# Performance work log

Measured on AMD Instinct MI355X. Metric: run time of the kernel, lower is better.

Reference implementation:

```python
import jax, jax.numpy as jnp
import numpy as np

L_RTN = 3  # complex taps produced by the RTN head (w_rtn3 out dim = 2*L_RTN)
EPS = 1e-12


def _to_complex(x):
    # (B, 2n) real interleaved [re0, im0, re1, im1, ...] -> (B, n) complex
    return x[:, 0::2] + 1j * x[:, 1::2]


def _to_real(xc):
    # (B, n) complex -> (B, 2n) real interleaved
    b, n = xc.shape
    return jnp.stack([xc.real, xc.imag], axis=-1).reshape(b, 2 * n)


def _complex_conv_taps(h_c, x_c):
    # per-sample causal complex FIR: out[t] = sum_l h[l] * x[t-l]
    # h_c: (B, L) complex, x_c: (B, n) complex
    n = x_c.shape[1]
    out = jnp.zeros_like(x_c)
    for l in range(h_c.shape[1]):  # L is tiny and static
        shifted = jnp.pad(x_c, ((0, 0), (l, 0)))[:, :n]
        out = out + h_c[:, l:l + 1] * shifted
    return out


def setup_inputs() -> dict:
    key = jax.random.key(0)
    ks = jax.random.split(key, 16)
    B, D_IN, H1, CH, H_RTN, H2, D_OUT = 8192, 512, 4096, 256, 1024, 4096, 512
    s = 0.02  # weight init scale
    x = jax.random.normal(ks[0], (B, D_IN), jnp.float32)
    w1 = s * jax.random.normal(ks[1], (H1, D_IN), jnp.float32)
    b1 = jnp.zeros((H1,), jnp.float32)
    w2 = s * jax.random.normal(ks[2], (CH, H1), jnp.float32)
    b2 = jnp.zeros((CH,), jnp.float32)
    w_rtn1 = s * jax.random.normal(ks[3], (H_RTN, CH), jnp.float32)
    b_rtn1 = jnp.zeros((H_RTN,), jnp.float32)
    w_rtn2 = s * jax.random.normal(ks[4], (H_RTN, H_RTN), jnp.float32)
    b_rtn2 = jnp.zeros((H_RTN,), jnp.float32)
    w_rtn3 = s * jax.random.normal(ks[5], (2 * L_RTN, H_RTN), jnp.float32)
    # bias so that RTN starts near identity tap [1, 0, 0, ...]
    b_rtn3 = jnp.zeros((2 * L_RTN,), jnp.float32).at[0].set(1.0)
    w3 = s * jax.random.normal(ks[6], (H2, CH), jnp.float32)
    b3 = jnp.zeros((H2,), jnp.float32)
    w4 = s * jax.random.normal(ks[7], (D_OUT, H2), jnp.float32)
    b4 = jnp.zeros((D_OUT,), jnp.float32)
    h = jax.random.normal(ks[8], (2,), jnp.float32)
    h = h / jnp.linalg.norm(h)  # unit-power single-tap fading channel
    noise = 0.1 * jax.random.normal(ks[9], (B, CH), jnp.float32)
    return {"x": x, "w1": w1, "b1": b1, "w2": w2, "b2": b2,
            "w_rtn1": w_rtn1, "b_rtn1": b_rtn1, "w_rtn2": w_rtn2,
            "b_rtn2": b_rtn2, "w_rtn3": w_rtn3, "b_rtn3": b_rtn3,
            "w3": w3, "b3": b3, "w4": w4, "b4": b4, "h": h, "noise": noise}


def reference(x, w1, b1, w2, b2, w_rtn1, b_rtn1, w_rtn2, b_rtn2,
              w_rtn3, b_rtn3, w3, b3, w4, b4, h, noise):
    # encoder (linear1 -> relu -> linear2)
    a = jax.nn.relu(x @ w1.T + b1)
    s = a @ w2.T + b2                      # (B, 2n) channel signal
    # power normalization: sqrt(2n) * sqrt(0.5) * s / ||s||
    scale = jnp.sqrt(s.shape[1] * 0.5)
    s = scale * s / jnp.linalg.norm(s, axis=1, keepdims=True)
    tx_c = _to_complex(s)                  # (B, n) transmitted symbols
    # single-tap complex channel
    h_c = h[0] + 1j * h[1]
    y = _to_real(h_c * tx_c) + noise       # add per-sample AWGN
    y_c = _to_complex(y)
    # LS channel estimate (1 tap): h_est = <y, x> / <x, x>
    num = jnp.sum(y_c * jnp.conj(tx_c), axis=1, keepdims=True)
    den = jnp.sum(jnp.abs(tx_c) ** 2, axis=1, keepdims=True)
    h_est = num / den                      # (B, 1)
    # zero-forcing signal estimate
    x_eq = y_c * jnp.conj(h_est) / (jnp.abs(h_est) ** 2 + EPS)
    xr = _to_real(x_eq)                    # (B, 2n)
    # RTN: predict inverse taps and apply per-sample complex conv
    g = jnp.tanh(xr @ w_rtn1.T + b_rtn1)
    g = jnp.tanh(g @ w_rtn2.T + b_rtn2)
    h_inv = g @ w_rtn3.T + b_rtn3          # (B, 2*L_RTN)
    h_inv_c = h_inv[:, 0::2] + 1j * h_inv[:, 1::2]
    xr = _to_real(_complex_conv_taps(h_inv_c, _to_complex(xr)))
    # decoder (linear3 -> relu -> linear4)
    out = jax.nn.relu(xr @ w3.T + b3)
    return out @ w4.T + b4
```

## Files before the change

### kernel.cpp

```cpp
#include <hip/hip_runtime.h>
#include <hip/hip_bf16.h>
#include <math.h>

using bf16 = __hip_bfloat16;
typedef __attribute__((ext_vector_type(8))) short short8;
typedef __attribute__((ext_vector_type(4))) float float4v;

template <typename T> __device__ inline T cvt_out(float v);
template <> __device__ inline float cvt_out<float>(float v) { return v; }
template <> __device__ inline bf16 cvt_out<bf16>(float v) { return __float2bfloat16(v); }

__device__ inline void gload_lds16(const bf16* g, bf16* l) {
    __builtin_amdgcn_global_load_lds(
        (const __attribute__((address_space(1))) void*)g,
        (__attribute__((address_space(3))) void*)l, 16, 0, 0);
}

struct CvtPack {
    const float* src[7];
    bf16* dst[7];
    int end[7];
};

__global__ __launch_bounds__(256) void cvt_all(CvtPack p) {
    int e = (blockIdx.x * 256 + threadIdx.x) * 4;
    int start = 0;
#pragma unroll
    for (int s = 0; s < 7; ++s) {
        if (e < p.end[s]) {
            int off = e - start;
            float4 v = *(const float4*)(p.src[s] + off);
            bf16* d = p.dst[s] + off;
            d[0] = __float2bfloat16(v.x);
            d[1] = __float2bfloat16(v.y);
            d[2] = __float2bfloat16(v.z);
            d[3] = __float2bfloat16(v.w);
            return;
        }
        start = p.end[s];
    }
}

__device__ inline float4 load4f(const float* p) { return *(const float4*)p; }
__device__ inline float4 load4f(const bf16* p) {
    ushort4 u = *(const ushort4*)p;
    float4 r;
    r.x = __uint_as_float((unsigned)u.x << 16);
    r.y = __uint_as_float((unsigned)u.y << 16);
    r.z = __uint_as_float((unsigned)u.z << 16);
    r.w = __uint_as_float((unsigned)u.w << 16);
    return r;
}
__device__ inline void store4(float* p, float4 v) { *(float4*)p = v; }
__device__ inline void store4(bf16* p, float4 v) {
    p[0] = __float2bfloat16(v.x); p[1] = __float2bfloat16(v.y);
    p[2] = __float2bfloat16(v.z); p[3] = __float2bfloat16(v.w);
}

template <int NK, int ACT, typename InT, typename OutT>
__global__ __launch_bounds__(256) void reduceK(const InT* __restrict__ p,
                                               const float* __restrict__ bias,
                                               OutT* __restrict__ out,
                                               size_t mn, int nmask, int total4) {
    int i = blockIdx.x * 256 + threadIdx.x;
    if (i < total4) {
        int idx = i * 4;
        float4 r = *(const float4*)(bias + (idx & nmask));
#pragma unroll
        for (int k = 0; k < NK; ++k) {
            float4 a = load4f(p + k * mn + idx);
            r.x += a.x; r.y += a.y; r.z += a.z; r.w += a.w;
        }
        if (ACT == 1) {
            r.x = fmaxf(r.x, 0.f); r.y = fmaxf(r.y, 0.f);
            r.z = fmaxf(r.z, 0.f); r.w = fmaxf(r.w, 0.f);
        } else if (ACT == 2) {
            r.x = tanhf(r.x); r.y = tanhf(r.y);
            r.z = tanhf(r.z); r.w = tanhf(r.w);
        }
        store4(out + idx, r);
    }
}

template <int ACT, typename OutT, int WMT, int WNT, int BKT, bool PARTIAL>
__global__ __launch_bounds__(256) void gemm_bt(const bf16* __restrict__ A,
                                               const bf16* __restrict__ W,
                                               const float* __restrict__ bias,
                                               OutT* __restrict__ C,
                                               int M, int N, int K,
                                               int nbn, int kcount) {
    constexpr int TBM = 32 * WMT;
    constexpr int TBN = 32 * WNT;
    constexpr int CPR = BKT / 8;
    constexpr int CA = TBM * CPR;
    constexpr int CB = TBN * CPR;

    __shared__ bf16 As[TBM * BKT];
    __shared__ bf16 Bs[TBN * BKT];

    const int bi = blockIdx.x;
    const int xcd = bi & 7, t = bi >> 3;
    const int bn = t % nbn;
    const int bm = xcd + 8 * (t / nbn);
    const int kbeg = PARTIAL ? blockIdx.y * kcount : 0;
    OutT* Cp = PARTIAL ? C + (size_t)blockIdx.y * M * N : C;

    const int tid = threadIdx.x;
    const int wave = tid >> 6, lane = tid & 63;
    const int wm = (wave >> 1) * (16 * WMT), wn = (wave & 1) * (16 * WNT);
    const int quad = lane >> 4, lrow = lane & 15;

    float4v acc[WMT][WNT] = {};
    const size_t arow = (size_t)(bm * TBM) * K;
    const size_t brow = (size_t)(bn * TBN) * K;

    for (int k0 = kbeg; k0 < kbeg + kcount; k0 += BKT) {
        __syncthreads();
#pragma unroll
        for (int tt = 0; tt < CA / 256; ++tt) {
            int base = tt * 256 + wave * 64;
            int c = base + lane;
            int row = c / CPR, col = (c % CPR) * 8;
            gload_lds16(A + arow + (size_t)row * K + k0 + col, As + base * 8);
        }
#pragma unroll
        for (int tt = 0; tt < CB / 256; ++tt) {
            int base = tt * 256 + wave * 64;
            int c = base + lane;
            int row = c / CPR, col = (c % CPR) * 8;
            gload_lds16(W + brow + (size_t)row * K + k0 + col, Bs + base * 8);
        }
        __syncthreads();
#pragma unroll
        for (int kk = 0; kk < BKT; kk += 32) {
            short8 af[WMT], bfr[WNT];
#pragma unroll
            for (int i = 0; i < WMT; ++i)
                af[i] = *(const short8*)(As + (wm + i * 16 + lrow) * BKT + kk + quad * 8);
#pragma unroll
            for (int j = 0; j < WNT; ++j)
                bfr[j] = *(const short8*)(Bs + (wn + j * 16 + lrow) * BKT + kk + quad * 8);
#pragma unroll
            for (int i = 0; i < WMT; ++i)
#pragma unroll
                for (int j = 0; j < WNT; ++j)
                    acc[i][j] = __builtin_amdgcn_mfma_f32_16x16x32_bf16(af[i], bfr[j], acc[i][j], 0, 0, 0);
        }
    }

#pragma unroll
    for (int i = 0; i < WMT; ++i) {
        int m0 = bm * TBM + wm + i * 16 + quad * 4;
#pragma unroll
        for (int j = 0; j < WNT; ++j) {
            int n = bn * TBN + wn + j * 16 + lrow;
            if constexpr (PARTIAL) {
#pragma unroll
                for (int r = 0; r < 4; ++r)
                    Cp[(size_t)(m0 + r) * N + n] = cvt_out<OutT>(acc[i][j][r]);
            } else {
                float bv = bias[n];
#pragma unroll
                for (int r = 0; r < 4; ++r) {
                    float v = acc[i][j][r] + bv;
                    if (ACT == 1) v = fmaxf(v, 0.f);
                    else if (ACT == 2) v = tanhf(v);
                    Cp[(size_t)(m0 + r) * N + n] = cvt_out<OutT>(v);
                }
            }
        }
    }
}

template <int ACT, typename OutT>
__global__ __launch_bounds__(512, 4) void gemm_bt_wide(const bf16* __restrict__ A,
                                                       const bf16* __restrict__ W,
                                                       const float* __restrict__ bias,
                                                       OutT* __restrict__ C,
                                                       int M, int N, int K,
                                                       int nbn) {
    constexpr int TBM = 256, TBN = 128, BKT = 64;
    constexpr int CPR = BKT / 8;
    constexpr int CA = TBM * CPR;
    constexpr int CB = TBN * CPR;

    __shared__ bf16 As[TBM * BKT];
    __shared__ bf16 Bs[TBN * BKT];

    const int bi = blockIdx.x;
    const int xcd = bi & 7, t = bi >> 3;
    const int bn = t % nbn;
    const int bm = xcd + 8 * (t / nbn);

    const int tid = threadIdx.x;
    const int wave = tid >> 6, lane = tid & 63;
    const int wm = (wave >> 1) * 64, wn = (wave & 1) * 64;
    const int quad = lane >> 4, lrow = lane & 15;

    float4v acc[4][4] = {};
    const size_t arow = (size_t)(bm * TBM) * K;
    const size_t brow = (size_t)(bn * TBN) * K;

    for (int k0 = 0; k0 < K; k0 += BKT) {
        __syncthreads();
#pragma unroll
        for (int tt = 0; tt < CA / 512; ++tt) {
            int base = tt * 512 + wave * 64;
            int c = base + lane;
            int row = c / CPR, col = (c % CPR) * 8;
            gload_lds16(A + arow + (size_t)row * K + k0 + col, As + base * 8);
        }
#pragma unroll
        for (int tt = 0; tt < CB / 512; ++tt) {
            int base = tt * 512 + wave * 64;
            int c = base + lane;
            int row = c / CPR, col = (c % CPR) * 8;
            gload_lds16(W + brow + (size_t)row * K + k0 + col, Bs + base * 8);
        }
        __syncthreads();
#pragma unroll
        for (int kk = 0; kk < BKT; kk += 32) {
            short8 af[4], bfr[4];
#pragma unroll
            for (int i = 0; i < 4; ++i)
                af[i] = *(const short8*)(As + (wm + i * 16 + lrow) * BKT + kk + quad * 8);
#pragma unroll
            for (int j = 0; j < 4; ++j)
                bfr[j] = *(const short8*)(Bs + (wn + j * 16 + lrow) * BKT + kk + quad * 8);
#pragma unroll
            for (int i = 0; i < 4; ++i)
#pragma unroll
                for (int j = 0; j < 4; ++j)
                    acc[i][j] = __builtin_amdgcn_mfma_f32_16x16x32_bf16(af[i], bfr[j], acc[i][j], 0, 0, 0);
        }
    }

#pragma unroll
    for (int i = 0; i < 4; ++i) {
        int m0 = bm * TBM + wm + i * 16 + quad * 4;
#pragma unroll
        for (int j = 0; j < 4; ++j) {
            int n = bn * TBN + wn + j * 16 + lrow;
            float bv = bias[n];
#pragma unroll
            for (int r = 0; r < 4; ++r) {
                float v = acc[i][j][r] + bv;
                if (ACT == 1) v = fmaxf(v, 0.f);
                else if (ACT == 2) v = tanhf(v);
                C[(size_t)(m0 + r) * N + n] = cvt_out<OutT>(v);
            }
        }
    }
}

__global__ __launch_bounds__(64) void channel_kernel(const float* __restrict__ s,
                                                     const float* __restrict__ h,
                                                     const float* __restrict__ noise,
                                                     float* __restrict__ xr_f,
                                                     bf16* __restrict__ xr_b) {
    const int b = blockIdx.x, lane = threadIdx.x;
    const float* srow = s + (size_t)b * 256;

    float ss = 0.f;
#pragma unroll
    for (int t = 0; t < 4; ++t) {
        float v = srow[lane + 64 * t];
        ss += v * v;
    }
#pragma unroll
    for (int off = 32; off; off >>= 1) ss += __shfl_xor(ss, off);
    const float inv = sqrtf(128.0f) / sqrtf(ss);

    const float hre = h[0], him = h[1];

    float yre[2], yim[2];
    float nre = 0.f, nim = 0.f, den = 0.f;
#pragma unroll
    for (int t = 0; t < 2; ++t) {
        int c = lane + 64 * t;
        float tr = srow[2 * c] * inv, ti = srow[2 * c + 1] * inv;
        float yr = hre * tr - him * ti + noise[(size_t)b * 256 + 2 * c];
        float yi = hre * ti + him * tr + noise[(size_t)b * 256 + 2 * c + 1];
        yre[t] = yr; yim[t] = yi;
        nre += yr * tr + yi * ti;
        nim += yi * tr - yr * ti;
        den += tr * tr + ti * ti;
    }
#pragma unroll
    for (int off = 32; off; off >>= 1) {
        nre += __shfl_xor(nre, off);
        nim += __shfl_xor(nim, off);
        den += __shfl_xor(den, off);
    }
    const float her = nre / den, hei = nim / den;
    const float d2 = her * her + hei * hei + 1e-12f;

#pragma unroll
    for (int t = 0; t < 2; ++t) {
        int c = lane + 64 * t;
        float xre = (yre[t] * her + yim[t] * hei) / d2;
        float xim = (yim[t] * her - yre[t] * hei) / d2;
        xr_f[(size_t)b * 256 + 2 * c] = xre;
        xr_f[(size_t)b * 256 + 2 * c + 1] = xim;
        xr_b[(size_t)b * 256 + 2 * c] = __float2bfloat16(xre);
        xr_b[(size_t)b * 256 + 2 * c + 1] = __float2bfloat16(xim);
    }
}

__global__ __launch_bounds__(64) void rtn_taps_conv(const bf16* __restrict__ g2,
                                                    const float* __restrict__ wr3,
                                                    const float* __restrict__ br3,
                                                    const float* __restrict__ xr_f,
                                                    bf16* __restrict__ xr2) {
    const int b = blockIdx.x, lane = threadIdx.x;
    const bf16* grow = g2 + (size_t)b * 1024;

    float acc[6] = {0.f, 0.f, 0.f, 0.f, 0.f, 0.f};
#pragma unroll
    for (int t = 0; t < 16; ++t) {
        int k = lane + 64 * t;
        float gv = __bfloat162float(grow[k]);
#pragma unroll
        for (int j = 0; j < 6; ++j) acc[j] += gv * wr3[j * 1024 + k];
    }
#pragma unroll
    for (int j = 0; j < 6; ++j)
#pragma unroll
        for (int off = 32; off; off >>= 1) acc[j] += __shfl_xor(acc[j], off);

    float tre[3], tim[3];
#pragma unroll
    for (int l = 0; l < 3; ++l) {
        tre[l] = acc[2 * l] + br3[2 * l];
        tim[l] = acc[2 * l + 1] + br3[2 * l + 1];
    }

    const float* xrow = xr_f + (size_t)b * 256;
#pragma unroll
    for (int t = 0; t < 2; ++t) {
        int c = lane + 64 * t;
        float ore = 0.f, oim = 0.f;
#pragma unroll
        for (int l = 0; l < 3; ++l) {
            int cc = c - l;
            if (cc >= 0) {
                float xre = xrow[2 * cc], xim = xrow[2 * cc + 1];
                ore += tre[l] * xre - tim[l] * xim;
                oim += tre[l] * xim + tim[l] * xre;
            }
        }
        xr2[(size_t)b * 256 + 2 * c] = __float2bfloat16(ore);
        xr2[(size_t)b * 256 + 2 * c + 1] = __float2bfloat16(oim);
    }
}

extern "C" void kernel_launch(void* const* d_in, const int* in_sizes, int n_in,
                              void* d_out, int out_size, void* d_ws, size_t ws_size,
                              hipStream_t stream) {
    constexpr int B = 8192, D_IN = 512, H1 = 4096, CH = 256, HR = 1024, H2 = 4096, DOUT = 512;

    const float* x   = (const float*)d_in[0];
    const float* w1  = (const float*)d_in[1];
    const float* b1  = (const float*)d_in[2];
    const float* w2  = (const float*)d_in[3];
    const float* b2  = (const float*)d_in[4];
    const float* wr1 = (const float*)d_in[5];
    const float* br1 = (const float*)d_in[6];
    const float* wr2 = (const float*)d_in[7];
    const float* br2 = (const float*)d_in[8];
    const float* wr3 = (const float*)d_in[9];
    const float* br3 = (const float*)d_in[10];
    const float* w3  = (const float*)d_in[11];
    const float* b3  = (const float*)d_in[12];
    const float* w4  = (const float*)d_in[13];
    const float* b4  = (const float*)d_in[14];
    const float* h   = (const float*)d_in[15];
    const float* noise = (const float*)d_in[16];

    char* ws = (char*)d_ws;
    bf16*  a    = (bf16*)(ws + 0);
    float* sF   = (float*)(ws + 0);
    bf16*  g1   = (bf16*)(ws + 0);
    bf16*  g2   = (bf16*)(ws + 16777216);
    bf16*  tbuf = (bf16*)(ws + 0);
    bf16*  w1B  = (bf16*)(ws + 67108864);
    bf16*  w2B  = (bf16*)(ws + 71303168);
    bf16*  wr1B = (bf16*)(ws + 73400320);
    bf16*  wr2B = (bf16*)(ws + 73924608);
    bf16*  w3B  = (bf16*)(ws + 76021760);
    bf16*  w4B  = (bf16*)(ws + 78118912);
    bf16*  xB   = (bf16*)(ws + 82313216);
    bf16*  g2P  = (bf16*)(ws + 82313216);
    float* xrF  = (float*)(ws + 99090432);
    bf16*  xrB  = (bf16*)(ws + 107479040);
    bf16*  xr2  = (bf16*)(ws + 111673344);
    bf16*  g6P  = (bf16*)(ws + 82313216);

    dim3 blk(256);

    CvtPack p;
    const float* srcs[7] = {x, w1, w2, wr1, wr2, w3, w4};
    bf16* dsts[7] = {xB, w1B, w2B, wr1B, wr2B, w3B, w4B};
    int ns[7] = {B * D_IN, H1 * D_IN, CH * H1, HR * CH, HR * HR, H2 * CH, DOUT * H2};
    int cum = 0;
    for (int i = 0; i < 7; ++i) { p.src[i] = srcs[i]; p.dst[i] = dsts[i]; cum += ns[i]; p.end[i] = cum; }
    cvt_all<<<(cum / 4 + 255) / 256, blk, 0, stream>>>(p);

    gemm_bt_wide<1, bf16><<<32 * 32, dim3(512), 0, stream>>>(
        xB, w1B, b1, a, B, H1, D_IN, 32);
    gemm_bt<0, bf16, 4, 2, 64, true><<<dim3(64 * 4, 4), blk, 0, stream>>>(
        a, w2B, nullptr, g2P, B, CH, H1, 4, H1 / 4);
    reduceK<4, 0, bf16, float><<<(B * CH / 4 + 255) / 256, blk, 0, stream>>>(
        g2P, b2, sF, (size_t)B * CH, CH - 1, B * CH / 4);
    channel_kernel<<<B, 64, 0, stream>>>(sF, h, noise, xrF, xrB);
    gemm_bt<2, bf16, 4, 2, 64, false><<<64 * 16, blk, 0, stream>>>(
        xrB, wr1B, br1, g1, B, HR, CH, 16, CH);
    gemm_bt<2, bf16, 4, 2, 64, false><<<64 * 16, blk, 0, stream>>>(
        g1, wr2B, br2, g2, B, HR, HR, 16, HR);
    rtn_taps_conv<<<B, 64, 0, stream>>>(g2, wr3, br3, xrF, xr2);
    gemm_bt_wide<1, bf16><<<32 * 32, dim3(512), 0, stream>>>(
        xr2, w3B, b3, tbuf, B, H2, CH, 32);
    gemm_bt<0, bf16, 4, 4, 64, true><<<dim3(64 * 4, 4), blk, 0, stream>>>(
        tbuf, w4B, nullptr, g6P, B, DOUT, H2, 4, H2 / 4);
    reduceK<4, 0, bf16, float><<<(B * DOUT / 4 + 255) / 256, blk, 0, stream>>>(
        g6P, b4, (float*)d_out, (size_t)B * DOUT, DOUT - 1, B * DOUT / 4);
}
```

Measured before the change: 364.4 us.

## Add double-buffered 256x256 swizzled-LDS GEMM for the four large layers

Introduces gemm_pipe, a 512-thread GEMM with 256x256 block tiles, double-buffered LDS filled by global_load_lds, an XOR swizzle on LDS columns to avoid bank conflicts, and s_setprio around the MFMA burst. It replaces the wide and split-K kernels for linear1/2/3/4 and changes the split-K factors (8 for linear2, 4 for linear4). The aim is to hide global-load latency behind MFMA work and to raise arithmetic intensity per tile. The cost is 128 KB of LDS per block, which allows fewer resident blocks, plus a larger register footprint for the 8x4 accumulator array. The second GEMM layer now gets only 256 blocks.

```diff
diff --git a/kernel.cpp b/kernel.cpp
--- a/kernel.cpp
+++ b/kernel.cpp
@@ -79,6 +79,122 @@
             r.z = tanhf(r.z); r.w = tanhf(r.w);
         }
         store4(out + idx, r);
+    }
+}
+
+template <int ACT, typename OutT, bool PARTIAL>
+__global__ __launch_bounds__(512, 2) void gemm_pipe(const bf16* __restrict__ A,
+                                                    const bf16* __restrict__ W,
+                                                    const float* __restrict__ bias,
+                                                    OutT* __restrict__ C,
+                                                    int M, int N, int K,
+                                                    int nbn, int kcount) {
+    __shared__ bf16 As[2][256 * 64];
+    __shared__ bf16 Bs[2][256 * 64];
+
+    const int bi = blockIdx.x;
+    const int xcd = bi & 7, t = bi >> 3;
+    const int bn = t % nbn;
+    const int bm = xcd + 8 * (t / nbn);
+    const int kbeg = PARTIAL ? blockIdx.y * kcount : 0;
+    OutT* Cp = PARTIAL ? C + (size_t)blockIdx.y * M * N : C;
+
+    const int tid = threadIdx.x;
+    const int wave = tid >> 6, lane = tid & 63;
+    const int wm = (wave >> 2) * 128, wn = (wave & 3) * 64;
+    const int quad = lane >> 4, lrow = lane & 15;
+
+    const bf16* Ab0 = A + (size_t)(bm * 256) * K + kbeg;
+    const bf16* Wb0 = W + (size_t)(bn * 256) * K + kbeg;
+
+    auto stage = [&](int kt, int bsel) {
+        const int k0 = kt * 64;
+#pragma unroll
+        for (int tt = 0; tt < 4; ++tt) {
+            int base = tt * 512 + wave * 64;
+            int c = base + lane;
+            int row = c >> 3, ch = c & 7;
+            gload_lds16(Ab0 + (size_t)row * K + k0 + ((ch ^ (row & 7)) << 3),
+                        &As[bsel][0] + base * 8);
+        }
+#pragma unroll
+        for (int tt = 0; tt < 4; ++tt) {
+            int base = tt * 512 + wave * 64;
+            int c = base + lane;
+            int row = c >> 3, ch = c & 7;
+            gload_lds16(Wb0 + (size_t)row * K + k0 + ((ch ^ (row & 7)) << 3),
+                        &Bs[bsel][0] + base * 8);
+        }
+    };
+
+    float4v acc[8][4] = {};
+    const int NT = kcount >> 6;
+
+    stage(0, 0);
+    if (NT > 1) {
+        stage(1, 1);
+        asm volatile("s_waitcnt vmcnt(8)" ::: "memory");
+    } else {
+        asm volatile("s_waitcnt vmcnt(0)" ::: "memory");
+    }
+    __builtin_amdgcn_s_barrier();
+
+    const int swz = lrow & 7;
+    for (int kt = 0; kt < NT; ++kt) {
+        const bf16* Ap = &As[kt & 1][0];
+        const bf16* Bp = &Bs[kt & 1][0];
+        short8 af[2][8], bfr[2][4];
+#pragma unroll
+        for (int ks = 0; ks < 2; ++ks) {
+            const int cswz = (((ks * 4 + quad) ^ swz) << 3);
+#pragma unroll
+            for (int i = 0; i < 8; ++i)
+                af[ks][i] = *(const short8*)(Ap + (wm + i * 16 + lrow) * 64 + cswz);
+#pragma unroll
+            for (int j = 0; j < 4; ++j)
+                bfr[ks][j] = *(const short8*)(Bp + (wn + j * 16 + lrow) * 64 + cswz);
+        }
+        asm volatile("s_waitcnt lgkmcnt(0)" ::: "memory");
+        __builtin_amdgcn_s_barrier();
+        if (kt + 2 < NT) stage(kt + 2, kt & 1);
+        __builtin_amdgcn_s_setprio(1);
+#pragma unroll
+        for (int ks = 0; ks < 2; ++ks)
+#pragma unroll
+            for (int i = 0; i < 8; ++i)
+#pragma unroll
+                for (int j = 0; j < 4; ++j)
+                    acc[i][j] = __builtin_amdgcn_mfma_f32_16x16x32_bf16(
+                        af[ks][i], bfr[ks][j], acc[i][j], 0, 0, 0);
+        __builtin_amdgcn_s_setprio(0);
+        if (kt + 1 < NT) {
+            if (kt + 2 < NT) asm volatile("s_waitcnt vmcnt(8)" ::: "memory");
+            else             asm volatile("s_waitcnt vmcnt(0)" ::: "memory");
+            __builtin_amdgcn_s_barrier();
+        }
+    }
+
+#pragma unroll
+    for (int i = 0; i < 8; ++i) {
+        int m0 = bm * 256 + wm + i * 16 + quad * 4;
+#pragma unroll
+        for (int j = 0; j < 4; ++j) {
+            int n = bn * 256 + wn + j * 16 + lrow;
+            if constexpr (PARTIAL) {
+#pragma unroll
+                for (int r = 0; r < 4; ++r)
+                    Cp[(size_t)(m0 + r) * N + n] = cvt_out<OutT>(acc[i][j][r]);
+            } else {
+                float bv = bias[n];
+#pragma unroll
+                for (int r = 0; r < 4; ++r) {
+                    float v = acc[i][j][r] + bv;
+                    if (ACT == 1) v = fmaxf(v, 0.f);
+                    else if (ACT == 2) v = tanhf(v);
+                    Cp[(size_t)(m0 + r) * N + n] = cvt_out<OutT>(v);
+                }
+            }
+        }
     }
 }
 
@@ -167,87 +283,6 @@
                     else if (ACT == 2) v = tanhf(v);
                     Cp[(size_t)(m0 + r) * N + n] = cvt_out<OutT>(v);
                 }
-            }
-        }
-    }
-}
-
-template <int ACT, typename OutT>
-__global__ __launch_bounds__(512, 4) void gemm_bt_wide(const bf16* __restrict__ A,
-                                                       const bf16* __restrict__ W,
-                                                       const float* __restrict__ bias,
-                                                       OutT* __restrict__ C,
-                                                       int M, int N, int K,
-                                                       int nbn) {
-    constexpr int TBM = 256, TBN = 128, BKT = 64;
-    constexpr int CPR = BKT / 8;
-    constexpr int CA = TBM * CPR;
-    constexpr int CB = TBN * CPR;
-
-    __shared__ bf16 As[TBM * BKT];
-    __shared__ bf16 Bs[TBN * BKT];
-
-    const int bi = blockIdx.x;
-    const int xcd = bi & 7, t = bi >> 3;
-    const int bn = t % nbn;
-    const int bm = xcd + 8 * (t / nbn);
-
-    const int tid = threadIdx.x;
-    const int wave = tid >> 6, lane = tid & 63;
-    const int wm = (wave >> 1) * 64, wn = (wave & 1) * 64;
-    const int quad = lane >> 4, lrow = lane & 15;
-
-    float4v acc[4][4] = {};
-    const size_t arow = (size_t)(bm * TBM) * K;
-    const size_t brow = (size_t)(bn * TBN) * K;
-
-    for (int k0 = 0; k0 < K; k0 += BKT) {
-        __syncthreads();
-#pragma unroll
-        for (int tt = 0; tt < CA / 512; ++tt) {
-            int base = tt * 512 + wave * 64;
-            int c = base + lane;
-            int row = c / CPR, col = (c % CPR) * 8;
-            gload_lds16(A + arow + (size_t)row * K + k0 + col, As + base * 8);
-        }
-#pragma unroll
-        for (int tt = 0; tt < CB / 512; ++tt) {
-            int base = tt * 512 + wave * 64;
-            int c = base + lane;
-            int row = c / CPR, col = (c % CPR) * 8;
-            gload_lds16(W + brow + (size_t)row * K + k0 + col, Bs + base * 8);
-        }
-        __syncthreads();
-#pragma unroll
-        for (int kk = 0; kk < BKT; kk += 32) {
-            short8 af[4], bfr[4];
-#pragma unroll
-            for (int i = 0; i < 4; ++i)
-                af[i] = *(const short8*)(As + (wm + i * 16 + lrow) * BKT + kk + quad * 8);
-#pragma unroll
-            for (int j = 0; j < 4; ++j)
-                bfr[j] = *(const short8*)(Bs + (wn + j * 16 + lrow) * BKT + kk + quad * 8);
-#pragma unroll
-            for (int i = 0; i < 4; ++i)
-#pragma unroll
-                for (int j = 0; j < 4; ++j)
-                    acc[i][j] = __builtin_amdgcn_mfma_f32_16x16x32_bf16(af[i], bfr[j], acc[i][j], 0, 0, 0);
-        }
-    }
-
-#pragma unroll
-    for (int i = 0; i < 4; ++i) {
-        int m0 = bm * TBM + wm + i * 16 + quad * 4;
-#pragma unroll
-        for (int j = 0; j < 4; ++j) {
-            int n = bn * TBN + wn + j * 16 + lrow;
-            float bv = bias[n];
-#pragma unroll
-            for (int r = 0; r < 4; ++r) {
-                float v = acc[i][j][r] + bv;
-                if (ACT == 1) v = fmaxf(v, 0.f);
-                else if (ACT == 2) v = tanhf(v);
-                C[(size_t)(m0 + r) * N + n] = cvt_out<OutT>(v);
             }
         }
     }
@@ -406,11 +441,11 @@
     for (int i = 0; i < 7; ++i) { p.src[i] = srcs[i]; p.dst[i] = dsts[i]; cum += ns[i]; p.end[i] = cum; }
     cvt_all<<<(cum / 4 + 255) / 256, blk, 0, stream>>>(p);
 
-    gemm_bt_wide<1, bf16><<<32 * 32, dim3(512), 0, stream>>>(
-        xB, w1B, b1, a, B, H1, D_IN, 32);
-    gemm_bt<0, bf16, 4, 2, 64, true><<<dim3(64 * 4, 4), blk, 0, stream>>>(
-        a, w2B, nullptr, g2P, B, CH, H1, 4, H1 / 4);
-    reduceK<4, 0, bf16, float><<<(B * CH / 4 + 255) / 256, blk, 0, stream>>>(
+    gemm_pipe<1, bf16, false><<<dim3(32 * 16), dim3(512), 0, stream>>>(
+        xB, w1B, b1, a, B, H1, D_IN, 16, D_IN);
+    gemm_pipe<0, bf16, true><<<dim3(32, 8), dim3(512), 0, stream>>>(
+        a, w2B, nullptr, g2P, B, CH, H1, 1, H1 / 8);
+    reduceK<8, 0, bf16, float><<<(B * CH / 4 + 255) / 256, blk, 0, stream>>>(
         g2P, b2, sF, (size_t)B * CH, CH - 1, B * CH / 4);
     channel_kernel<<<B, 64, 0, stream>>>(sF, h, noise, xrF, xrB);
     gemm_bt<2, bf16, 4, 2, 64, false><<<64 * 16, blk, 0, stream>>>(
@@ -418,10 +453,10 @@
     gemm_bt<2, bf16, 4, 2, 64, false><<<64 * 16, blk, 0, stream>>>(
         g1, wr2B, br2, g2, B, HR, HR, 16, HR);
     rtn_taps_conv<<<B, 64, 0, stream>>>(g2, wr3, br3, xrF, xr2);
-    gemm_bt_wide<1, bf16><<<32 * 32, dim3(512), 0, stream>>>(
-        xr2, w3B, b3, tbuf, B, H2, CH, 32);
-    gemm_bt<0, bf16, 4, 4, 64, true><<<dim3(64 * 4, 4), blk, 0, stream>>>(
-        tbuf, w4B, nullptr, g6P, B, DOUT, H2, 4, H2 / 4);
+    gemm_pipe<1, bf16, false><<<dim3(32 * 16), dim3(512), 0, stream>>>(
+        xr2, w3B, b3, tbuf, B, H2, CH, 16, CH);
+    gemm_pipe<0, bf16, true><<<dim3(32 * 2, 4), dim3(512), 0, stream>>>(
+        tbuf, w4B, nullptr, g6P, B, DOUT, H2, 2, H2 / 4);
     reduceK<4, 0, bf16, float><<<(B * DOUT / 4 + 255) / 256, blk, 0, stream>>>(
         g6P, b4, (float*)d_out, (size_t)B * DOUT, DOUT - 1, B * DOUT / 4);
 }
```

Measured after the change: 342.0 us. -6.2%, faster.
